# Optimization experiments

Hardware: AMD Instinct MI355X
Metric: run time of the kernel (lower is better)

## Reference

```python
import jax, jax.numpy as jnp
import numpy as np

N, M, D = 16384, 4096, 512
TEMP = 1.0


def setup_inputs() -> dict:
    key = jax.random.key(0)
    kx, ky = jax.random.split(key)
    x = jax.random.normal(kx, (N, D), dtype=jnp.float32)
    y = jax.random.normal(ky, (M, D), dtype=jnp.float32)
    return {"x": x, "y": y, "temperature": 1}


def reference(x, y, temperature):
    # euclidean_distances_logits:
    #   logits = -0.5 * T * sum_d (x[n,None,:] - y[None,m,:])**2
    # Fused form avoiding the O(n*m*d) broadcast intermediate (same math):
    t = jnp.asarray(temperature, dtype=x.dtype) * jnp.float32(TEMP)
    x_sq = jnp.sum(x * x, axis=1, keepdims=True)          # [n, 1]
    y_sq = jnp.sum(y * y, axis=1)[None, :]                # [1, m]
    xy = jnp.einsum("nd,md->nm", x, y)                    # [n, m]
    sq_dist = x_sq - 2.0 * xy + y_sq                      # [n, m]
    return -0.5 * t * sq_dist
```

## Files before the change

### kernel.cpp

```cpp
#include <hip/hip_runtime.h>
#include <hip/hip_bf16.h>


#define NN 16384
#define MM 4096
#define DD 512

using frag_ab = __attribute__((ext_vector_type(8))) short;
using floatx4 = __attribute__((ext_vector_type(4))) float;

using gas_ptr = const __attribute__((address_space(1))) void*;
using las_ptr = __attribute__((address_space(3))) void*;

__device__ __forceinline__ void async_copy16(const void* g, void* l) {
    __builtin_amdgcn_global_load_lds((gas_ptr)g, (las_ptr)l, 16, 0, 0);
}

__device__ __forceinline__ unsigned bf16rne(float f) {
    union { float f; unsigned u; } v; v.f = f;
    unsigned u = v.u + 0x7FFFu + ((v.u >> 16) & 1u);
    return u >> 16;
}

__device__ __forceinline__ uint2 cvt4(float4 v) {
    uint2 r;
    r.x = bf16rne(v.x) | (bf16rne(v.y) << 16);
    r.y = bf16rne(v.z) | (bf16rne(v.w) << 16);
    return r;
}

__global__ void prep_kernel(const float* __restrict__ v, float* __restrict__ sq,
                            unsigned short* __restrict__ vb) {
    const int lane = threadIdx.x & 63;
    const int row  = blockIdx.x * 4 + (threadIdx.x >> 6);
    const float* p = v + (size_t)row * DD + lane * 8;
    float4 a = *(const float4*)(p);
    float4 b = *(const float4*)(p + 4);
    uint2 lo = cvt4(a), hi = cvt4(b);
    *(uint4*)(vb + (size_t)row * DD + lane * 8) = make_uint4(lo.x, lo.y, hi.x, hi.y);
    float s = a.x*a.x + a.y*a.y + a.z*a.z + a.w*a.w
            + b.x*b.x + b.y*b.y + b.z*b.z + b.w*b.w;
    #pragma unroll
    for (int off = 32; off > 0; off >>= 1) s += __shfl_xor(s, off);
    if (lane == 0) sq[row] = s;
}

__global__ void rowsq_kernel(const float* __restrict__ v, float* __restrict__ sq) {
    const int lane = threadIdx.x & 63;
    const int row  = blockIdx.x * 4 + (threadIdx.x >> 6);
    const float* p = v + (size_t)row * DD + lane * 8;
    float4 a = *(const float4*)(p);
    float4 b = *(const float4*)(p + 4);
    float s = a.x*a.x + a.y*a.y + a.z*a.z + a.w*a.w
            + b.x*b.x + b.y*b.y + b.z*b.z + b.w*b.w;
    #pragma unroll
    for (int off = 32; off > 0; off >>= 1) s += __shfl_xor(s, off);
    if (lane == 0) sq[row] = s;
}

__global__ __launch_bounds__(256) void protonet_gemm_bf(
    const unsigned short* __restrict__ xb, const unsigned short* __restrict__ yb,
    const float* __restrict__ xsq, const float* __restrict__ ysq,
    const int* __restrict__ temp, float* __restrict__ out)
{
    __shared__ __align__(16) unsigned short As[128 * 32];
    __shared__ __align__(16) unsigned short Bs[128 * 32];

    const int bn   = blockIdx.x;
    const int bm   = blockIdx.y;
    const int tid  = threadIdx.x;
    const int lane = tid & 63;
    const int wave = tid >> 6;
    const int wn   = wave & 1;
    const int wm   = wave >> 1;
    const int l15  = lane & 15;
    const int quad = lane >> 4;

    floatx4 acc[4][4] = {};

    const unsigned short* ga0 = xb + (size_t)(bn * 128 + (wave * 2 + 0) * 16 + l15) * DD + quad * 8;
    const unsigned short* ga1 = xb + (size_t)(bn * 128 + (wave * 2 + 1) * 16 + l15) * DD + quad * 8;
    const unsigned short* gb0 = yb + (size_t)(bm * 128 + (wave * 2 + 0) * 16 + l15) * DD + quad * 8;
    const unsigned short* gb1 = yb + (size_t)(bm * 128 + (wave * 2 + 1) * 16 + l15) * DD + quad * 8;

    for (int k0 = 0; k0 < DD; k0 += 32) {
        async_copy16(ga0 + k0, As + (wave * 2 + 0) * 512);
        async_copy16(ga1 + k0, As + (wave * 2 + 1) * 512);
        async_copy16(gb0 + k0, Bs + (wave * 2 + 0) * 512);
        async_copy16(gb1 + k0, Bs + (wave * 2 + 1) * 512);
        __syncthreads();

        frag_ab a[4], b[4];
        #pragma unroll
        for (int t = 0; t < 4; ++t) {
            a[t] = *(const frag_ab*)(As + (wn * 4 + t) * 512 + lane * 8);
            b[t] = *(const frag_ab*)(Bs + (wm * 4 + t) * 512 + lane * 8);
        }
        #pragma unroll
        for (int tn = 0; tn < 4; ++tn)
            #pragma unroll
            for (int tm = 0; tm < 4; ++tm)
                acc[tn][tm] = __builtin_amdgcn_mfma_f32_16x16x32_bf16(
                    a[tn], b[tm], acc[tn][tm], 0, 0, 0);
        __syncthreads();
    }

    const float t = (float)(*temp);
    const int n_base = bn * 128 + wn * 64;
    const int m_base = bm * 128 + wm * 64;
    #pragma unroll
    for (int tn = 0; tn < 4; ++tn) {
        float xs[4];
        #pragma unroll
        for (int r = 0; r < 4; ++r) xs[r] = xsq[n_base + tn * 16 + quad * 4 + r];
        #pragma unroll
        for (int tm = 0; tm < 4; ++tm) {
            const int mcol = m_base + tm * 16 + l15;
            const float ys = ysq[mcol];
            #pragma unroll
            for (int r = 0; r < 4; ++r) {
                const int nrow = n_base + tn * 16 + quad * 4 + r;
                out[(size_t)nrow * MM + mcol] = t * (acc[tn][tm][r] - 0.5f * (xs[r] + ys));
            }
        }
    }
}

__global__ __launch_bounds__(256) void protonet_gemm(
    const float* __restrict__ x, const float* __restrict__ y,
    const float* __restrict__ xsq, const float* __restrict__ ysq,
    const int* __restrict__ temp, float* __restrict__ out)
{
    __shared__ __align__(16) unsigned short As[128 * 32];
    __shared__ __align__(16) unsigned short Bs[128 * 32];

    const int bn   = blockIdx.x;
    const int bm   = blockIdx.y;
    const int tid  = threadIdx.x;
    const int lane = tid & 63;
    const int wave = tid >> 6;
    const int wn   = wave & 1;
    const int wm   = wave >> 1;
    const int l15  = lane & 15;
    const int quad = lane >> 4;

    floatx4 acc[4][4] = {};

    for (int k0 = 0; k0 < DD; k0 += 32) {
        #pragma unroll
        for (int i = 0; i < 4; ++i) {
            int c = tid + i * 256;
            int row = c >> 3, col4 = c & 7;
            float4 v = *(const float4*)(x + (size_t)(bn * 128 + row) * DD + k0 + col4 * 4);
            *(uint2*)(&As[row * 32 + col4 * 4]) = cvt4(v);
        }
        #pragma unroll
        for (int i = 0; i < 4; ++i) {
            int c = tid + i * 256;
            int row = c >> 3, col4 = c & 7;
            float4 v = *(const float4*)(y + (size_t)(bm * 128 + row) * DD + k0 + col4 * 4);
            *(uint2*)(&Bs[row * 32 + col4 * 4]) = cvt4(v);
        }
        __syncthreads();

        frag_ab a[4], b[4];
        #pragma unroll
        for (int t = 0; t < 4; ++t) {
            a[t] = *(const frag_ab*)(&As[(wn * 64 + t * 16 + l15) * 32 + quad * 8]);
            b[t] = *(const frag_ab*)(&Bs[(wm * 64 + t * 16 + l15) * 32 + quad * 8]);
        }
        #pragma unroll
        for (int tn = 0; tn < 4; ++tn)
            #pragma unroll
            for (int tm = 0; tm < 4; ++tm)
                acc[tn][tm] = __builtin_amdgcn_mfma_f32_16x16x32_bf16(
                    a[tn], b[tm], acc[tn][tm], 0, 0, 0);
        __syncthreads();
    }

    const float t = (float)(*temp);
    const int n_base = bn * 128 + wn * 64;
    const int m_base = bm * 128 + wm * 64;
    #pragma unroll
    for (int tn = 0; tn < 4; ++tn) {
        float xs[4];
        #pragma unroll
        for (int r = 0; r < 4; ++r) xs[r] = xsq[n_base + tn * 16 + quad * 4 + r];
        #pragma unroll
        for (int tm = 0; tm < 4; ++tm) {
            const int mcol = m_base + tm * 16 + l15;
            const float ys = ysq[mcol];
            #pragma unroll
            for (int r = 0; r < 4; ++r) {
                const int nrow = n_base + tn * 16 + quad * 4 + r;
                out[(size_t)nrow * MM + mcol] = t * (acc[tn][tm][r] - 0.5f * (xs[r] + ys));
            }
        }
    }
}

extern "C" void kernel_launch(void* const* d_in, const int* in_sizes, int n_in,
                              void* d_out, int out_size, void* d_ws, size_t ws_size,
                              hipStream_t stream) {
    const float* x    = (const float*)d_in[0];
    const float* y    = (const float*)d_in[1];
    const int*   temp = (const int*)d_in[2];
    float* out = (float*)d_out;

    float* xsq = (float*)d_ws;
    float* ysq = xsq + NN;
    unsigned short* xb = (unsigned short*)(ysq + MM);
    unsigned short* yb = xb + (size_t)NN * DD;

    const size_t need = (size_t)(NN + MM) * 4 + (size_t)(NN + MM) * DD * 2;

    if (ws_size >= need) {
        prep_kernel<<<NN / 4, 256, 0, stream>>>(x, xsq, xb);
        prep_kernel<<<MM / 4, 256, 0, stream>>>(y, ysq, yb);
        protonet_gemm_bf<<<dim3(NN / 128, MM / 128), 256, 0, stream>>>(
            xb, yb, xsq, ysq, temp, out);
    } else {
        rowsq_kernel<<<NN / 4, 256, 0, stream>>>(x, xsq);
        rowsq_kernel<<<MM / 4, 256, 0, stream>>>(y, ysq);
        protonet_gemm<<<dim3(NN / 128, MM / 128), 256, 0, stream>>>(
            x, y, xsq, ysq, temp, out);
    }
}
```

Measured before the change: 421.4 us.

## Use 256x256 double-buffered bf16 GEMM tile and merge prep kernels

Replaces the 128x128 single-buffered GEMM with a 512-thread 256x256 tile that has a 64-wide K step and double-buffered LDS. The next K slice is prefetched asynchronously while MFMAs run on the current one. This is meant to cut global/LDS traffic per flop, halve the barrier count, and overlap loads with compute. The two conversion/row-norm prep launches are merged into one kernel. The tile uses 128KB of LDS and 32 accumulators per wave, so occupancy drops and register pressure rises. With only 256 blocks, the grid may fill the GPU less well.

Measured after the change: 371.6 us. -11.8%, faster.

```diff
diff --git a/kernel.cpp b/kernel.cpp
--- a/kernel.cpp
+++ b/kernel.cpp
@@ -29,20 +29,30 @@
     return r;
 }
 
-__global__ void prep_kernel(const float* __restrict__ v, float* __restrict__ sq,
-                            unsigned short* __restrict__ vb) {
+__global__ void prep_all(const float* __restrict__ x, const float* __restrict__ y,
+                         float* __restrict__ xsq, float* __restrict__ ysq,
+                         unsigned short* __restrict__ xb, unsigned short* __restrict__ yb) {
     const int lane = threadIdx.x & 63;
     const int row  = blockIdx.x * 4 + (threadIdx.x >> 6);
-    const float* p = v + (size_t)row * DD + lane * 8;
+    const float* src;
+    unsigned short* db;
+    float* ds;
+    if (row < NN) {
+        src = x + (size_t)row * DD; db = xb + (size_t)row * DD; ds = xsq + row;
+    } else {
+        const int r = row - NN;
+        src = y + (size_t)r * DD; db = yb + (size_t)r * DD; ds = ysq + r;
+    }
+    const float* p = src + lane * 8;
     float4 a = *(const float4*)(p);
     float4 b = *(const float4*)(p + 4);
     uint2 lo = cvt4(a), hi = cvt4(b);
-    *(uint4*)(vb + (size_t)row * DD + lane * 8) = make_uint4(lo.x, lo.y, hi.x, hi.y);
+    *(uint4*)(db + lane * 8) = make_uint4(lo.x, lo.y, hi.x, hi.y);
     float s = a.x*a.x + a.y*a.y + a.z*a.z + a.w*a.w
             + b.x*b.x + b.y*b.y + b.z*b.z + b.w*b.w;
     #pragma unroll
     for (int off = 32; off > 0; off >>= 1) s += __shfl_xor(s, off);
-    if (lane == 0) sq[row] = s;
+    if (lane == 0) *ds = s;
 }
 
 __global__ void rowsq_kernel(const float* __restrict__ v, float* __restrict__ sq) {
@@ -58,8 +68,111 @@
     if (lane == 0) sq[row] = s;
 }
 
-__global__ __launch_bounds__(256) void protonet_gemm_bf(
+__global__ __launch_bounds__(512, 2) void protonet_gemm_256(
     const unsigned short* __restrict__ xb, const unsigned short* __restrict__ yb,
+    const float* __restrict__ xsq, const float* __restrict__ ysq,
+    const int* __restrict__ temp, float* __restrict__ out)
+{
+    __shared__ __align__(16) unsigned short S[65536];
+
+    const int bn   = blockIdx.x;
+    const int bm   = blockIdx.y;
+    const int tid  = threadIdx.x;
+    const int lane = tid & 63;
+    const int wave = tid >> 6;
+    const int wx   = wave >> 2;
+    const int wy   = wave & 3;
+    const int l15  = lane & 15;
+    const int quad = lane >> 4;
+
+    floatx4 acc[8][4] = {};
+
+    const unsigned short* gsrc[8];
+    int loff[8];
+    #pragma unroll
+    for (int c = 0; c < 8; ++c) {
+        const int s  = wave * 8 + c;
+        const int ss = s & 31;
+        const int rg = ss >> 1;
+        const int kh = ss & 1;
+        const bool a_side = (s < 32);
+        const unsigned short* base = a_side
+            ? xb + ((size_t)(bn * 256 + rg * 16 + l15) * DD + kh * 32 + quad * 8)
+            : yb + ((size_t)(bm * 256 + rg * 16 + l15) * DD + kh * 32 + quad * 8);
+        gsrc[c] = base;
+        loff[c] = (a_side ? 0 : 32768) + ss * 512;
+    }
+
+    #pragma unroll
+    for (int c = 0; c < 8; ++c)
+        async_copy16(gsrc[c], S + loff[c]);
+    __syncthreads();
+
+    for (int t = 0; t < 8; ++t) {
+        const int koff = (t & 1) * 16384;
+
+        if (t < 7) {
+            const int k0n = (t + 1) * 64;
+            const int pko = ((t + 1) & 1) * 16384;
+            #pragma unroll
+            for (int c = 0; c < 8; ++c)
+                async_copy16(gsrc[c] + k0n, S + (loff[c] + pko));
+        }
+        __builtin_amdgcn_sched_barrier(0);
+
+        frag_ab b[4][2];
+        #pragma unroll
+        for (int fc = 0; fc < 4; ++fc)
+            #pragma unroll
+            for (int kh = 0; kh < 2; ++kh)
+                b[fc][kh] = *(const frag_ab*)(S + 32768 + koff
+                                              + ((wy * 4 + fc) * 2 + kh) * 512 + lane * 8);
+
+        #pragma unroll
+        for (int pr = 0; pr < 4; ++pr) {
+            frag_ab a[2][2];
+            #pragma unroll
+            for (int i = 0; i < 2; ++i)
+                #pragma unroll
+                for (int kh = 0; kh < 2; ++kh)
+                    a[i][kh] = *(const frag_ab*)(S + koff
+                                  + ((wx * 8 + pr * 2 + i) * 2 + kh) * 512 + lane * 8);
+            #pragma unroll
+            for (int i = 0; i < 2; ++i)
+                #pragma unroll
+                for (int fc = 0; fc < 4; ++fc)
+                    #pragma unroll
+                    for (int kh = 0; kh < 2; ++kh)
+                        acc[pr * 2 + i][fc] = __builtin_amdgcn_mfma_f32_16x16x32_bf16(
+                            a[i][kh], b[fc][kh], acc[pr * 2 + i][fc], 0, 0, 0);
+        }
+
+        __syncthreads();
+    }
+
+    const float tt = (float)(*temp);
+    const int n_base = bn * 256 + wx * 128;
+    const int m_base = bm * 256 + wy * 64;
+    #pragma unroll
+    for (int fr = 0; fr < 8; ++fr) {
+        float xs[4];
+        #pragma unroll
+        for (int r = 0; r < 4; ++r) xs[r] = xsq[n_base + fr * 16 + quad * 4 + r];
+        #pragma unroll
+        for (int fc = 0; fc < 4; ++fc) {
+            const int mcol = m_base + fc * 16 + l15;
+            const float ys = ysq[mcol];
+            #pragma unroll
+            for (int r = 0; r < 4; ++r) {
+                const int nrow = n_base + fr * 16 + quad * 4 + r;
+                out[(size_t)nrow * MM + mcol] = tt * (acc[fr][fc][r] - 0.5f * (xs[r] + ys));
+            }
+        }
+    }
+}
+
+__global__ __launch_bounds__(256) void protonet_gemm(
+    const float* __restrict__ x, const float* __restrict__ y,
     const float* __restrict__ xsq, const float* __restrict__ ysq,
     const int* __restrict__ temp, float* __restrict__ out)
 {
@@ -78,74 +191,6 @@
 
     floatx4 acc[4][4] = {};
 
-    const unsigned short* ga0 = xb + (size_t)(bn * 128 + (wave * 2 + 0) * 16 + l15) * DD + quad * 8;
-    const unsigned short* ga1 = xb + (size_t)(bn * 128 + (wave * 2 + 1) * 16 + l15) * DD + quad * 8;
-    const unsigned short* gb0 = yb + (size_t)(bm * 128 + (wave * 2 + 0) * 16 + l15) * DD + quad * 8;
-    const unsigned short* gb1 = yb + (size_t)(bm * 128 + (wave * 2 + 1) * 16 + l15) * DD + quad * 8;
-
-    for (int k0 = 0; k0 < DD; k0 += 32) {
-        async_copy16(ga0 + k0, As + (wave * 2 + 0) * 512);
-        async_copy16(ga1 + k0, As + (wave * 2 + 1) * 512);
-        async_copy16(gb0 + k0, Bs + (wave * 2 + 0) * 512);
-        async_copy16(gb1 + k0, Bs + (wave * 2 + 1) * 512);
-        __syncthreads();
-
-        frag_ab a[4], b[4];
-        #pragma unroll
-        for (int t = 0; t < 4; ++t) {
-            a[t] = *(const frag_ab*)(As + (wn * 4 + t) * 512 + lane * 8);
-            b[t] = *(const frag_ab*)(Bs + (wm * 4 + t) * 512 + lane * 8);
-        }
-        #pragma unroll
-        for (int tn = 0; tn < 4; ++tn)
-            #pragma unroll
-            for (int tm = 0; tm < 4; ++tm)
-                acc[tn][tm] = __builtin_amdgcn_mfma_f32_16x16x32_bf16(
-                    a[tn], b[tm], acc[tn][tm], 0, 0, 0);
-        __syncthreads();
-    }
-
-    const float t = (float)(*temp);
-    const int n_base = bn * 128 + wn * 64;
-    const int m_base = bm * 128 + wm * 64;
-    #pragma unroll
-    for (int tn = 0; tn < 4; ++tn) {
-        float xs[4];
-        #pragma unroll
-        for (int r = 0; r < 4; ++r) xs[r] = xsq[n_base + tn * 16 + quad * 4 + r];
-        #pragma unroll
-        for (int tm = 0; tm < 4; ++tm) {
-            const int mcol = m_base + tm * 16 + l15;
-            const float ys = ysq[mcol];
-            #pragma unroll
-            for (int r = 0; r < 4; ++r) {
-                const int nrow = n_base + tn * 16 + quad * 4 + r;
-                out[(size_t)nrow * MM + mcol] = t * (acc[tn][tm][r] - 0.5f * (xs[r] + ys));
-            }
-        }
-    }
-}
-
-__global__ __launch_bounds__(256) void protonet_gemm(
-    const float* __restrict__ x, const float* __restrict__ y,
-    const float* __restrict__ xsq, const float* __restrict__ ysq,
-    const int* __restrict__ temp, float* __restrict__ out)
-{
-    __shared__ __align__(16) unsigned short As[128 * 32];
-    __shared__ __align__(16) unsigned short Bs[128 * 32];
-
-    const int bn   = blockIdx.x;
-    const int bm   = blockIdx.y;
-    const int tid  = threadIdx.x;
-    const int lane = tid & 63;
-    const int wave = tid >> 6;
-    const int wn   = wave & 1;
-    const int wm   = wave >> 1;
-    const int l15  = lane & 15;
-    const int quad = lane >> 4;
-
-    floatx4 acc[4][4] = {};
-
     for (int k0 = 0; k0 < DD; k0 += 32) {
         #pragma unroll
         for (int i = 0; i < 4; ++i) {
@@ -215,9 +260,8 @@
     const size_t need = (size_t)(NN + MM) * 4 + (size_t)(NN + MM) * DD * 2;
 
     if (ws_size >= need) {
-        prep_kernel<<<NN / 4, 256, 0, stream>>>(x, xsq, xb);
-        prep_kernel<<<MM / 4, 256, 0, stream>>>(y, ysq, yb);
-        protonet_gemm_bf<<<dim3(NN / 128, MM / 128), 256, 0, stream>>>(
+        prep_all<<<(NN + MM) / 4, 256, 0, stream>>>(x, y, xsq, ysq, xb, yb);
+        protonet_gemm_256<<<dim3(NN / 256, MM / 256), 512, 0, stream>>>(
             xb, yb, xsq, ysq, temp, out);
     } else {
         rowsq_kernel<<<NN / 4, 256, 0, stream>>>(x, xsq);
```
